# Optimization experiments

Measured on AMD Instinct MI355X. Metric: run time of the kernel, lower is better.

Reference implementation:

```python
import jax, jax.numpy as jnp
import numpy as np

EPS = 1e-6


def conv1x1(x, w, b):
    # x: [n,c,h,w], w: [o,c], b: [o]
    return jnp.einsum('nchw,oc->nohw', x, w) + b[None, :, None, None]


def maxpool2(x):
    n, c, h, w = x.shape
    return x.reshape(n, c, h // 2, 2, w // 2, 2).max(axis=(3, 5))


def resize_bilinear_ac(img, oh, ow):
    # bilinear resize with align_corners=True, img: [n,c,h,w]
    n, c, h, w = img.shape
    ys = jnp.linspace(0.0, h - 1.0, oh)
    xs = jnp.linspace(0.0, w - 1.0, ow)
    y0 = jnp.floor(ys).astype(jnp.int32)
    y1 = jnp.minimum(y0 + 1, h - 1)
    wy = (ys - y0.astype(img.dtype))
    x0 = jnp.floor(xs).astype(jnp.int32)
    x1 = jnp.minimum(x0 + 1, w - 1)
    wx = (xs - x0.astype(img.dtype))
    rows = img[:, :, y0, :] * (1.0 - wy)[None, None, :, None] + img[:, :, y1, :] * wy[None, None, :, None]
    return rows[:, :, :, x0] * (1.0 - wx)[None, None, None, :] + rows[:, :, :, x1] * wx[None, None, None, :]


def setup_inputs() -> dict:
    key = jax.random.key(0)
    ks = jax.random.split(key, 8)
    n, c, h, w = 4, 128, 256, 256
    ch = c // 2
    x = jax.random.normal(ks[0], (n, c, h, w), dtype=jnp.float32)
    depth_map = jax.random.uniform(ks[1], (n, 1, h, w), dtype=jnp.float32)
    s = 0.05
    return {
        'x': x,
        'depth_map': depth_map,
        'w_theta': jax.random.normal(ks[2], (ch, c), dtype=jnp.float32) * s,
        'b_theta': jnp.zeros((ch,), dtype=jnp.float32),
        'w_phi': jax.random.normal(ks[3], (ch, c), dtype=jnp.float32) * s,
        'b_phi': jnp.zeros((ch,), dtype=jnp.float32),
        'w_g': jax.random.normal(ks[4], (ch, c), dtype=jnp.float32) * s,
        'b_g': jnp.zeros((ch,), dtype=jnp.float32),
        'w_down': jnp.full((c, 1, 4, 4), 1.0 / 16.0, dtype=jnp.float32),  # depthwise 4x4 stride-4
        'w_z': jax.random.normal(ks[5], (c, ch), dtype=jnp.float32) * s,
        'b_z': jnp.zeros((c,), dtype=jnp.float32),
    }


def reference(x, depth_map, w_theta, b_theta, w_phi, b_phi, w_g, b_g, w_down, w_z, b_z):
    n, c, h, w = x.shape
    ch = c // 2
    # depthwise stride-4 downsample
    x_down = jax.lax.conv_general_dilated(
        x, w_down, window_strides=(4, 4), padding='VALID',
        feature_group_count=c, dimension_numbers=('NCHW', 'OIHW', 'NCHW'))
    # g, phi get extra 2x2 maxpool -> M = (h/8)*(w/8); theta stays at N = (h/4)*(w/4)
    g = maxpool2(conv1x1(x_down, w_g, b_g)).reshape(n, ch, -1).transpose(0, 2, 1)      # [n, M, ch]
    theta = conv1x1(x_down, w_theta, b_theta).reshape(n, ch, -1).transpose(0, 2, 1)    # [n, N, ch]
    phi = maxpool2(conv1x1(x_down, w_phi, b_phi)).reshape(n, ch, -1)                    # [n, ch, M]
    Ra = jax.nn.softmax(jnp.einsum('nic,ncj->nij', theta, phi), axis=2)                 # [n, N, M]
    # depth affinity
    d1 = resize_bilinear_ac(depth_map, h // 4, w // 4).reshape(n, -1, 1)                # [n, N, 1]
    d2 = resize_bilinear_ac(depth_map, h // 8, w // 8).reshape(n, 1, -1)                # [n, 1, M]
    Rd = jax.nn.softmax(jnp.minimum(d1 / (d2 + EPS), d2 / (d1 + EPS)), axis=2)          # [n, N, M]
    S = jax.nn.softmax(Ra * Rd, axis=2)
    y = jnp.einsum('nij,njc->nic', S, g).transpose(0, 2, 1).reshape(n, ch, h // 4, w // 4)
    return x + resize_bilinear_ac(conv1x1(y, w_z, b_z), h, w)
```

## Files before the change

### kernel.cpp

```cpp
#include <hip/hip_runtime.h>

#define EPSF 1e-6f

__device__ __forceinline__ float wave_max(float v) {
    #pragma unroll
    for (int m = 32; m; m >>= 1) v = fmaxf(v, __shfl_xor(v, m, 64));
    return v;
}
__device__ __forceinline__ float wave_sum(float v) {
    #pragma unroll
    for (int m = 32; m; m >>= 1) v += __shfl_xor(v, m, 64);
    return v;
}

__global__ void k_down(const float* __restrict__ x, const float* __restrict__ wd,
                       float* __restrict__ xd) {
    int idx = blockIdx.x * 256 + threadIdx.x;
    int ow = idx & 63;
    int oh = (idx >> 6) & 63;
    int c  = (idx >> 12) & 127;
    int n  = idx >> 19;
    const float* xp = x + ((((size_t)n * 128 + c) * 256 + oh * 4) * 256) + ow * 4;
    const float* w  = wd + c * 16;
    float acc = 0.f;
    #pragma unroll
    for (int r = 0; r < 4; ++r) {
        float4 v = *reinterpret_cast<const float4*>(xp + (size_t)r * 256);
        acc += w[r*4+0]*v.x + w[r*4+1]*v.y + w[r*4+2]*v.z + w[r*4+3]*v.w;
    }
    xd[idx] = acc;
}

__global__ void k_conv(const float* __restrict__ xd,
                       const float* __restrict__ w0, const float* __restrict__ b0,
                       const float* __restrict__ w1, const float* __restrict__ b1,
                       const float* __restrict__ w2, const float* __restrict__ b2,
                       float* __restrict__ theta, float* __restrict__ phi_u,
                       float* __restrict__ g_u) {
    __shared__ float wl[64 * 128];
    int which = blockIdx.z;
    const float* w = (which == 0) ? w0 : (which == 1) ? w1 : w2;
    const float* b = (which == 0) ? b0 : (which == 1) ? b1 : b2;
    float* out = (which == 0) ? theta : (which == 1) ? phi_u : g_u;
    for (int i = threadIdx.x; i < 64 * 128; i += 256) wl[i] = w[i];
    __syncthreads();
    int n = blockIdx.y;
    int p = blockIdx.x * 256 + threadIdx.x;
    const float* xp = xd + (size_t)n * 128 * 4096 + p;
    float acc[64];
    #pragma unroll
    for (int o = 0; o < 64; ++o) acc[o] = b[o];
    for (int c = 0; c < 128; ++c) {
        float xv = xp[(size_t)c * 4096];
        #pragma unroll
        for (int o = 0; o < 64; ++o) acc[o] = fmaf(wl[o * 128 + c], xv, acc[o]);
    }
    float* op = out + (size_t)n * 64 * 4096 + p;
    #pragma unroll
    for (int o = 0; o < 64; ++o) op[(size_t)o * 4096] = acc[o];
}

__global__ void k_pool(const float* __restrict__ phi_u, const float* __restrict__ g_u,
                       float* __restrict__ phi, float* __restrict__ g_t) {
    int idx = blockIdx.x * 256 + threadIdx.x;
    int q = idx & 1023;
    int o = (idx >> 10) & 63;
    int n = idx >> 16;
    int qh = q >> 5, qw = q & 31;
    const float* sel = (blockIdx.y == 0) ? phi_u : g_u;
    const float* sp = sel + (((size_t)n * 64 + o) * 4096) + (qh * 2) * 64 + qw * 2;
    float m = fmaxf(fmaxf(sp[0], sp[1]), fmaxf(sp[64], sp[65]));
    if (blockIdx.y == 0) phi[idx] = m;
    else g_t[((size_t)n * 1024 + q) * 64 + o] = m;
}

__global__ void k_d12(const float* __restrict__ depth, float* __restrict__ d1,
                      float* __restrict__ d2) {
    int idx = blockIdx.x * 256 + threadIdx.x;
    const int T1 = 4 * 4096;
    bool is1 = idx < T1;
    int e = is1 ? idx : idx - T1;
    if (!is1 && e >= 4 * 1024) return;
    int n, oh, ow;
    float fy, fx;
    if (is1) { n = e >> 12; oh = (e >> 6) & 63; ow = e & 63;
               fy = (oh * 255.f) / 63.f;  fx = (ow * 255.f) / 63.f; }
    else     { n = e >> 10; oh = (e >> 5) & 31; ow = e & 31;
               fy = (oh * 255.f) / 31.f;  fx = (ow * 255.f) / 31.f; }
    int y0 = (int)floorf(fy); int y1 = min(y0 + 1, 255);
    int x0 = (int)floorf(fx); int x1 = min(x0 + 1, 255);
    float wy = fy - (float)y0, wx = fx - (float)x0;
    const float* dp = depth + (size_t)n * 65536;
    float v00 = dp[y0 * 256 + x0], v01 = dp[y0 * 256 + x1];
    float v10 = dp[y1 * 256 + x0], v11 = dp[y1 * 256 + x1];
    float r0 = v00 * (1.f - wx) + v01 * wx;
    float r1 = v10 * (1.f - wx) + v11 * wx;
    float v  = r0 * (1.f - wy) + r1 * wy;
    if (is1) d1[e] = v; else d2[e] = v;
}

#define ROWS 16
#define RPW  4
#define CCH  16
__global__ __launch_bounds__(256, 1)
void k_attn(const float* __restrict__ theta, const float* __restrict__ phi,
            const float* __restrict__ g_t, const float* __restrict__ d1,
            const float* __restrict__ d2, float* __restrict__ y_t) {
    __shared__ float sbuf[CCH * 1024];
    __shared__ float gbuf[256 * 64];
    __shared__ float thl[64 * ROWS];
    __shared__ float d2l[1024];

    int n = blockIdx.y;
    int row0 = blockIdx.x * ROWS;
    int tid = threadIdx.x;
    int lane = tid & 63;
    int wv = tid >> 6;

    for (int i = tid; i < ROWS * 64; i += 256) {
        int r = i & (ROWS - 1); int c = i >> 4;
        thl[c * ROWS + r] = theta[((size_t)n * 64 + c) * 4096 + row0 + r];
    }
    for (int i = tid; i < 1024; i += 256) d2l[i] = d2[n * 1024 + i];

    float acc[RPW][16];
    #pragma unroll
    for (int r = 0; r < RPW; ++r)
        #pragma unroll
        for (int k = 0; k < 16; ++k) acc[r][k] = 0.f;

    for (int cc = 0; cc < 64; cc += CCH) {
        __syncthreads();
        for (int i = tid; i < CCH * 1024; i += 256)
            sbuf[i] = phi[((size_t)n * 64 + cc) * 1024 + i];
        __syncthreads();
        #pragma unroll
        for (int c = 0; c < CCH; ++c) {
            float ph[16];
            #pragma unroll
            for (int k = 0; k < 16; ++k) ph[k] = sbuf[c * 1024 + k * 64 + lane];
            #pragma unroll
            for (int r = 0; r < RPW; ++r) {
                float th = thl[(cc + c) * ROWS + wv * RPW + r];
                #pragma unroll
                for (int k = 0; k < 16; ++k) acc[r][k] = fmaf(th, ph[k], acc[r][k]);
            }
        }
    }

    float d2v[16], d2inv[16];
    #pragma unroll
    for (int k = 0; k < 16; ++k) {
        d2v[k] = d2l[k * 64 + lane];
        d2inv[k] = 1.f / (d2v[k] + EPSF);
    }
    float yscale[RPW];
    #pragma unroll
    for (int r = 0; r < RPW; ++r) {
        float m = -1e30f;
        #pragma unroll
        for (int k = 0; k < 16; ++k) m = fmaxf(m, acc[r][k]);
        m = wave_max(m);
        float sum = 0.f;
        #pragma unroll
        for (int k = 0; k < 16; ++k) { float e = __expf(acc[r][k] - m); acc[r][k] = e; sum += e; }
        sum = wave_sum(sum);
        float inv_ra = 1.f / sum;
        float d1v = d1[n * 4096 + row0 + wv * RPW + r];
        float inv1 = 1.f / (d1v + EPSF);
        float rdl[16];
        float dm = -1e30f;
        #pragma unroll
        for (int k = 0; k < 16; ++k) {
            float v = fminf(d1v * d2inv[k], d2v[k] * inv1);
            rdl[k] = v; dm = fmaxf(dm, v);
        }
        dm = wave_max(dm);
        float dsum = 0.f;
        #pragma unroll
        for (int k = 0; k < 16; ++k) { float e = __expf(rdl[k] - dm); rdl[k] = e; dsum += e; }
        dsum = wave_sum(dsum);
        float inv = inv_ra / dsum;
        float pm = -1e30f;
        #pragma unroll
        for (int k = 0; k < 16; ++k) { float p = acc[r][k] * rdl[k] * inv; acc[r][k] = p; pm = fmaxf(pm, p); }
        pm = wave_max(pm);
        float ss = 0.f;
        #pragma unroll
        for (int k = 0; k < 16; ++k) { float e = __expf(acc[r][k] - pm); acc[r][k] = e; ss += e; }
        ss = wave_sum(ss);
        yscale[r] = 1.f / ss;
    }

    __syncthreads();
    #pragma unroll
    for (int r = 0; r < RPW; ++r)
        #pragma unroll
        for (int k = 0; k < 16; ++k)
            sbuf[(wv * RPW + r) * 1024 + k * 64 + lane] = acc[r][k];

    float yacc[RPW];
    #pragma unroll
    for (int r = 0; r < RPW; ++r) yacc[r] = 0.f;
    for (int jc = 0; jc < 1024; jc += 256) {
        __syncthreads();
        for (int i = tid; i < 256 * 64; i += 256)
            gbuf[i] = g_t[((size_t)n * 1024 + jc) * 64 + i];
        __syncthreads();
        #pragma unroll 4
        for (int j = 0; j < 256; ++j) {
            float gv = gbuf[j * 64 + lane];
            #pragma unroll
            for (int r = 0; r < RPW; ++r)
                yacc[r] = fmaf(sbuf[(wv * RPW + r) * 1024 + jc + j], gv, yacc[r]);
        }
    }
    #pragma unroll
    for (int r = 0; r < RPW; ++r)
        y_t[((size_t)n * 64 + lane) * 4096 + row0 + wv * RPW + r] = yacc[r] * yscale[r];
}

__global__ void k_z(const float* __restrict__ y_t, const float* __restrict__ w_z,
                    const float* __restrict__ b_z, float* __restrict__ z) {
    __shared__ float wl[64 * 64];
    int ohalf = blockIdx.z;
    for (int i = threadIdx.x; i < 64 * 64; i += 256)
        wl[i] = w_z[(size_t)(ohalf * 64) * 64 + i];
    __syncthreads();
    int n = blockIdx.y;
    int p = blockIdx.x * 256 + threadIdx.x;
    float acc[64];
    #pragma unroll
    for (int o = 0; o < 64; ++o) acc[o] = b_z[ohalf * 64 + o];
    const float* yp = y_t + (size_t)n * 64 * 4096 + p;
    for (int c = 0; c < 64; ++c) {
        float yv = yp[(size_t)c * 4096];
        #pragma unroll
        for (int o = 0; o < 64; ++o) acc[o] = fmaf(wl[o * 64 + c], yv, acc[o]);
    }
    float* zp = z + ((size_t)n * 128 + ohalf * 64) * 4096 + p;
    #pragma unroll
    for (int o = 0; o < 64; ++o) zp[(size_t)o * 4096] = acc[o];
}

__global__ void k_final(const float* __restrict__ x, const float* __restrict__ z,
                        float* __restrict__ out) {
    int idx = blockIdx.x * 256 + threadIdx.x;
    int j4 = idx & 63;
    int i  = (idx >> 6) & 255;
    int c  = (idx >> 14) & 127;
    int n  = idx >> 21;
    float fy = (i * 63.f) / 255.f;
    int y0 = (int)floorf(fy); int y1 = min(y0 + 1, 63);
    float wy = fy - (float)y0;
    const float* zp = z + ((size_t)n * 128 + c) * 4096;
    float4 xo = reinterpret_cast<const float4*>(x)[idx];
    float res[4];
    #pragma unroll
    for (int m = 0; m < 4; ++m) {
        int j = j4 * 4 + m;
        float fx = (j * 63.f) / 255.f;
        int x0 = (int)floorf(fx); int x1 = min(x0 + 1, 63);
        float wx = fx - (float)x0;
        float r0 = zp[y0 * 64 + x0] * (1.f - wx) + zp[y0 * 64 + x1] * wx;
        float r1 = zp[y1 * 64 + x0] * (1.f - wx) + zp[y1 * 64 + x1] * wx;
        res[m] = r0 * (1.f - wy) + r1 * wy;
    }
    float4 o;
    o.x = xo.x + res[0]; o.y = xo.y + res[1];
    o.z = xo.z + res[2]; o.w = xo.w + res[3];
    reinterpret_cast<float4*>(out)[idx] = o;
}

extern "C" void kernel_launch(void* const* d_in, const int* in_sizes, int n_in,
                              void* d_out, int out_size, void* d_ws, size_t ws_size,
                              hipStream_t stream) {
    const float* x       = (const float*)d_in[0];
    const float* depth   = (const float*)d_in[1];
    const float* w_theta = (const float*)d_in[2];
    const float* b_theta = (const float*)d_in[3];
    const float* w_phi   = (const float*)d_in[4];
    const float* b_phi   = (const float*)d_in[5];
    const float* w_g     = (const float*)d_in[6];
    const float* b_g     = (const float*)d_in[7];
    const float* w_down  = (const float*)d_in[8];
    const float* w_z     = (const float*)d_in[9];
    const float* b_z     = (const float*)d_in[10];
    float* out = (float*)d_out;

    float* ws = (float*)d_ws;
    float* xd    = ws;
    float* theta = xd    + 2097152;
    float* phi_u = theta + 1048576;
    float* g_u   = phi_u + 1048576;
    float* phi   = g_u   + 1048576;
    float* g_t   = phi   + 262144;
    float* d1    = g_t   + 262144;
    float* d2    = d1    + 16384;
    float* y_t   = d2    + 4096;
    float* z     = y_t   + 1048576;

    k_down <<<8192, 256, 0, stream>>>(x, w_down, xd);
    k_conv <<<dim3(16, 4, 3), 256, 0, stream>>>(xd, w_theta, b_theta, w_phi, b_phi,
                                                w_g, b_g, theta, phi_u, g_u);
    k_pool <<<dim3(1024, 2), 256, 0, stream>>>(phi_u, g_u, phi, g_t);
    k_d12  <<<80, 256, 0, stream>>>(depth, d1, d2);
    k_attn <<<dim3(256, 4), 256, 0, stream>>>(theta, phi, g_t, d1, d2, y_t);
    k_z    <<<dim3(16, 4, 2), 256, 0, stream>>>(y_t, w_z, b_z, z);
    k_final<<<32768, 256, 0, stream>>>(x, z, out);
}
```

Before: 715.0 us.

## Cut attention kernel LDS use: readlane broadcast of probabilities, direct g loads

The S·g product in the attention kernel now broadcasts each softmax probability from registers with readlane instead of writing S to shared memory, and reads g straight from global memory (L1/L2 cached) instead of staging it in LDS. The phi staging chunk is halved and copied with float4 loads, and launch bounds now ask for 3 blocks per CU. LDS drops from about 132KB to about 40KB so more blocks can be resident. The cost is a readlane per FMA group, uncoalesced-but-shared global g reads, and tighter register pressure under the higher occupancy bound.

Result: slower. 769.4 us (+7.6%).

```diff
diff --git a/kernel.cpp b/kernel.cpp
--- a/kernel.cpp
+++ b/kernel.cpp
@@ -11,6 +11,9 @@
     #pragma unroll
     for (int m = 32; m; m >>= 1) v += __shfl_xor(v, m, 64);
     return v;
+}
+__device__ __forceinline__ float lane_bcast(float v, int src) {
+    return __int_as_float(__builtin_amdgcn_readlane(__float_as_int(v), src));
 }
 
 __global__ void k_down(const float* __restrict__ x, const float* __restrict__ wd,
@@ -101,13 +104,12 @@
 
 #define ROWS 16
 #define RPW  4
-#define CCH  16
-__global__ __launch_bounds__(256, 1)
+#define CCH  8
+__global__ __launch_bounds__(256, 3)
 void k_attn(const float* __restrict__ theta, const float* __restrict__ phi,
             const float* __restrict__ g_t, const float* __restrict__ d1,
             const float* __restrict__ d2, float* __restrict__ y_t) {
-    __shared__ float sbuf[CCH * 1024];
-    __shared__ float gbuf[256 * 64];
+    __shared__ float pbuf[CCH * 1024];
     __shared__ float thl[64 * ROWS];
     __shared__ float d2l[1024];
 
@@ -131,14 +133,17 @@
 
     for (int cc = 0; cc < 64; cc += CCH) {
         __syncthreads();
-        for (int i = tid; i < CCH * 1024; i += 256)
-            sbuf[i] = phi[((size_t)n * 64 + cc) * 1024 + i];
+        {
+            const float4* src = reinterpret_cast<const float4*>(phi + ((size_t)n * 64 + cc) * 1024);
+            float4* dst = reinterpret_cast<float4*>(pbuf);
+            for (int i = tid; i < CCH * 256; i += 256) dst[i] = src[i];
+        }
         __syncthreads();
         #pragma unroll
         for (int c = 0; c < CCH; ++c) {
             float ph[16];
             #pragma unroll
-            for (int k = 0; k < 16; ++k) ph[k] = sbuf[c * 1024 + k * 64 + lane];
+            for (int k = 0; k < 16; ++k) ph[k] = pbuf[c * 1024 + k * 64 + lane];
             #pragma unroll
             for (int r = 0; r < RPW; ++r) {
                 float th = thl[(cc + c) * ROWS + wv * RPW + r];
@@ -192,27 +197,16 @@
         yscale[r] = 1.f / ss;
     }
 
-    __syncthreads();
-    #pragma unroll
-    for (int r = 0; r < RPW; ++r)
-        #pragma unroll
-        for (int k = 0; k < 16; ++k)
-            sbuf[(wv * RPW + r) * 1024 + k * 64 + lane] = acc[r][k];
-
-    float yacc[RPW];
-    #pragma unroll
-    for (int r = 0; r < RPW; ++r) yacc[r] = 0.f;
-    for (int jc = 0; jc < 1024; jc += 256) {
-        __syncthreads();
-        for (int i = tid; i < 256 * 64; i += 256)
-            gbuf[i] = g_t[((size_t)n * 1024 + jc) * 64 + i];
-        __syncthreads();
+    const float* gp = g_t + (size_t)n * 1024 * 64 + lane;
+    float yacc[RPW] = {0.f, 0.f, 0.f, 0.f};
+    #pragma unroll
+    for (int k = 0; k < 16; ++k) {
         #pragma unroll 4
-        for (int j = 0; j < 256; ++j) {
-            float gv = gbuf[j * 64 + lane];
+        for (int jj = 0; jj < 64; ++jj) {
+            float gv = gp[(size_t)(k * 64 + jj) * 64];
             #pragma unroll
             for (int r = 0; r < RPW; ++r)
-                yacc[r] = fmaf(sbuf[(wv * RPW + r) * 1024 + jc + j], gv, yacc[r]);
+                yacc[r] = fmaf(lane_bcast(acc[r][k], jj), gv, yacc[r]);
         }
     }
     #pragma unroll
```
